# Kernel tuning notes

Measured on AMD Instinct MI355X. Metric: run time of the kernel, lower is better.

## Reference

```python
import jax, jax.numpy as jnp
import numpy as np

D_K = 64


def setup_inputs() -> dict:
    key = jax.random.key(0)
    kq, kk, kv = jax.random.split(key, 3)
    B, H, S, D = 2, 16, 2048, D_K
    Q = jax.random.normal(kq, (B, H, S, D), dtype=jnp.float32)
    K = jax.random.normal(kk, (B, H, S, D), dtype=jnp.float32)
    V = jax.random.normal(kv, (B, H, S, D), dtype=jnp.float32)
    # causal mask: True = masked out (matches torch masked_fill_ semantics)
    causal = ~jnp.tril(jnp.ones((S, S), dtype=bool))
    attn_mask = jnp.broadcast_to(causal, (B, 1, S, S))
    return {"Q": Q, "K": K, "V": V, "attn_mask": attn_mask}


def reference(Q, K, V, attn_mask):
    # scores = Q K^T / sqrt(d_k), masked positions -> -1e9, softmax, then A V
    scale = 1.0 / np.sqrt(D_K).astype(np.float32)
    scores = jnp.einsum("bhqd,bhkd->bhqk", Q, K) * scale
    scores = jnp.where(attn_mask, jnp.float32(-1e9), scores)
    attn = jax.nn.softmax(scores, axis=-1)
    context = jnp.einsum("bhqk,bhkd->bhqd", attn, V)
    return (context, attn)
```

## Files before the change

kernel.cpp:

```cpp
#include <hip/hip_runtime.h>

typedef _Float16 half8  __attribute__((ext_vector_type(8)));
typedef _Float16 half4v __attribute__((ext_vector_type(4)));
typedef float    f32x4  __attribute__((ext_vector_type(4)));

#define S_LEN  2048
#define D_HEAD 64
#define TQ     16
#define EBS    2056

static __device__ __forceinline__ half8 cvt8(float4 a, float4 b) {
    half8 h;
    h[0] = (_Float16)a.x; h[1] = (_Float16)a.y; h[2] = (_Float16)a.z; h[3] = (_Float16)a.w;
    h[4] = (_Float16)b.x; h[5] = (_Float16)b.y; h[6] = (_Float16)b.z; h[7] = (_Float16)b.w;
    return h;
}

__global__ void prep_k(const float* __restrict__ K, _Float16* __restrict__ Kh, int n8) {
    int i = blockIdx.x * blockDim.x + threadIdx.x;
    if (i < n8) {
        const float4* p = (const float4*)K + (size_t)i * 2;
        ((half8*)Kh)[i] = cvt8(p[0], p[1]);
    }
}

__global__ void prep_vt(const float* __restrict__ V, _Float16* __restrict__ Vt) {
    __shared__ _Float16 lt[D_HEAD][136];
    const int bh = blockIdx.y;
    const int k0 = blockIdx.x * 128;
    const int t  = threadIdx.x;
    {
        const int kk = t >> 1, hf = t & 1;
        const float* vp = V + (size_t)bh * S_LEN * D_HEAD + (size_t)(k0 + kk) * D_HEAD + hf * 32;
#pragma unroll
        for (int j = 0; j < 8; ++j) {
            float4 a = *(const float4*)(vp + j * 4);
            lt[hf * 32 + j * 4 + 0][kk] = (_Float16)a.x;
            lt[hf * 32 + j * 4 + 1][kk] = (_Float16)a.y;
            lt[hf * 32 + j * 4 + 2][kk] = (_Float16)a.z;
            lt[hf * 32 + j * 4 + 3][kk] = (_Float16)a.w;
        }
    }
    __syncthreads();
    {
        const int d = t >> 2, kq = t & 3;
        _Float16* dst = Vt + ((size_t)bh * D_HEAD + d) * S_LEN + k0 + kq * 32;
        const half8* src = (const half8*)&lt[d][kq * 32];
#pragma unroll
        for (int j = 0; j < 4; ++j) ((half8*)dst)[j] = src[j];
    }
}

template <bool USE_WS>
__global__ __launch_bounds__(256, 2)
void sdpa_main(const float* __restrict__ Q, const float* __restrict__ K,
               const _Float16* __restrict__ Kh, const float* __restrict__ V,
               const _Float16* __restrict__ Vt, float* __restrict__ ctx,
               float* __restrict__ attn) {
    __shared__ __align__(16) _Float16 ebuf[TQ][EBS];
    __shared__ float rowsum[TQ];
    __shared__ float inv_l[TQ];

    const int tid  = threadIdx.x;
    const int wave = tid >> 6;
    const int lane = tid & 63;
    const int c    = lane & 15;
    const int quad = lane >> 4;

    const int qt = blockIdx.x;
    const int bh = blockIdx.y;
    const int q0 = qt * TQ;
    const int n_k   = q0 + TQ;
    const int n_t16 = n_k >> 4;
    const int n_c32 = (n_k + 31) >> 5;

    const size_t base = (size_t)bh * (S_LEN * D_HEAD);

    if (tid < TQ) rowsum[tid] = 0.0f;
    if (n_k & 31) {
        int r = tid >> 4, kk = n_k + (tid & 15);
        ebuf[r][kk] = (_Float16)0.0f;
    }

    half8 qf0, qf1;
    {
        const float* qp = Q + base + (size_t)(q0 + c) * D_HEAD + quad * 8;
        qf0 = cvt8(*(const float4*)qp, *(const float4*)(qp + 4));
        qf1 = cvt8(*(const float4*)(qp + 32), *(const float4*)(qp + 36));
    }
    __syncthreads();

    float psum = 0.0f;
    for (int t = wave; t < n_t16; t += 4) {
        const int k0 = t * 16;
        half8 kf0, kf1;
        if (USE_WS) {
            const _Float16* kp = Kh + base + (size_t)(k0 + c) * D_HEAD + quad * 8;
            kf0 = *(const half8*)kp;
            kf1 = *(const half8*)(kp + 32);
        } else {
            const float* kp = K + base + (size_t)(k0 + c) * D_HEAD + quad * 8;
            kf0 = cvt8(*(const float4*)kp, *(const float4*)(kp + 4));
            kf1 = cvt8(*(const float4*)(kp + 32), *(const float4*)(kp + 36));
        }
        f32x4 s = {0.0f, 0.0f, 0.0f, 0.0f};
        s = __builtin_amdgcn_mfma_f32_16x16x32_f16(kf0, qf0, s, 0, 0, 0);
        s = __builtin_amdgcn_mfma_f32_16x16x32_f16(kf1, qf1, s, 0, 0, 0);

        half4v ev;
#pragma unroll
        for (int r = 0; r < 4; ++r) {
            const int kg = k0 + quad * 4 + r;
            float e = (kg <= q0 + c) ? __expf(s[r] * 0.125f) : 0.0f;
            psum += e;
            ev[r] = (_Float16)e;
        }
        *(half4v*)&ebuf[c][k0 + quad * 4] = ev;
    }
    psum += __shfl_xor(psum, 16);
    psum += __shfl_xor(psum, 32);
    if (lane < 16) atomicAdd(&rowsum[c], psum);
    __syncthreads();
    if (tid < TQ) inv_l[tid] = 1.0f / rowsum[tid];

    f32x4 cacc = {0.0f, 0.0f, 0.0f, 0.0f};
    if (USE_WS) {
        const _Float16* vb = Vt + ((size_t)bh * D_HEAD + wave * 16 + c) * S_LEN;
        for (int chk = 0; chk < n_c32; ++chk) {
            const int k0 = chk * 32;
            half8 af = *(const half8*)&ebuf[c][k0 + quad * 8];
            half8 bf = *(const half8*)(vb + k0 + quad * 8);
            cacc = __builtin_amdgcn_mfma_f32_16x16x32_f16(af, bf, cacc, 0, 0, 0);
        }
    } else {
        for (int chk = 0; chk < n_c32; ++chk) {
            const int k0 = chk * 32;
            half8 af = *(const half8*)&ebuf[c][k0 + quad * 8];
            half8 bf;
#pragma unroll
            for (int j = 0; j < 8; ++j)
                bf[j] = (_Float16)V[base + (size_t)(k0 + quad * 8 + j) * D_HEAD + wave * 16 + c];
            cacc = __builtin_amdgcn_mfma_f32_16x16x32_f16(af, bf, cacc, 0, 0, 0);
        }
    }
    __syncthreads();

    {
        const int r  = tid >> 4;
        const int qg = q0 + r;
        const float il = inv_l[r];
        float* row = attn + (size_t)bh * S_LEN * S_LEN + (size_t)(q0 + r) * S_LEN;
#pragma unroll
        for (int it = 0; it < 16; ++it) {
            const int k8 = (tid & 15) * 8 + it * 128;
            float4 o0, o1;
            if (k8 + 7 <= qg) {
                half8 e = *(const half8*)&ebuf[r][k8];
                o0.x = (float)e[0] * il; o0.y = (float)e[1] * il;
                o0.z = (float)e[2] * il; o0.w = (float)e[3] * il;
                o1.x = (float)e[4] * il; o1.y = (float)e[5] * il;
                o1.z = (float)e[6] * il; o1.w = (float)e[7] * il;
            } else if (k8 > qg) {
                o0.x = o0.y = o0.z = o0.w = 0.0f;
                o1 = o0;
            } else {
                half8 e = *(const half8*)&ebuf[r][k8];
                o0.x = (k8 + 0 <= qg) ? (float)e[0] * il : 0.0f;
                o0.y = (k8 + 1 <= qg) ? (float)e[1] * il : 0.0f;
                o0.z = (k8 + 2 <= qg) ? (float)e[2] * il : 0.0f;
                o0.w = (k8 + 3 <= qg) ? (float)e[3] * il : 0.0f;
                o1.x = (k8 + 4 <= qg) ? (float)e[4] * il : 0.0f;
                o1.y = (k8 + 5 <= qg) ? (float)e[5] * il : 0.0f;
                o1.z = (k8 + 6 <= qg) ? (float)e[6] * il : 0.0f;
                o1.w = (k8 + 7 <= qg) ? (float)e[7] * il : 0.0f;
            }
            *(float4*)(row + k8)     = o0;
            *(float4*)(row + k8 + 4) = o1;
        }
    }

#pragma unroll
    for (int r = 0; r < 4; ++r) {
        const int qr = quad * 4 + r;
        ctx[base + (size_t)(q0 + qr) * D_HEAD + wave * 16 + c] = cacc[r] * inv_l[qr];
    }
}

extern "C" void kernel_launch(void* const* d_in, const int* in_sizes, int n_in,
                              void* d_out, int out_size, void* d_ws, size_t ws_size,
                              hipStream_t stream) {
    const float* Q = (const float*)d_in[0];
    const float* K = (const float*)d_in[1];
    const float* V = (const float*)d_in[2];

    const int BH = in_sizes[0] / (S_LEN * D_HEAD);
    float* ctx  = (float*)d_out;
    float* attn = (float*)d_out + (size_t)in_sizes[0];

    const size_t nKV  = (size_t)in_sizes[1];
    const size_t need = 2 * nKV * sizeof(_Float16);

    dim3 grid(S_LEN / TQ, BH);
    if (ws_size >= need) {
        _Float16* Kh = (_Float16*)d_ws;
        _Float16* Vt = Kh + nKV;
        prep_k<<<(int)((nKV / 8 + 255) / 256), 256, 0, stream>>>(K, Kh, (int)(nKV / 8));
        prep_vt<<<dim3(S_LEN / 128, BH), 256, 0, stream>>>(V, Vt);
        sdpa_main<true><<<grid, 256, 0, stream>>>(Q, K, Kh, V, Vt, ctx, attn);
    } else {
        sdpa_main<false><<<grid, 256, 0, stream>>>(Q, K, nullptr, V, nullptr, ctx, attn);
    }
}
```

Before: 744.9 us.

## Fuse K/V prep, schedule heavy tiles first, interleave PV MFMA with attn stores

Merges the K conversion and V transpose prep kernels into one launch. Remaps the flattened grid so the longest causal query tiles start first, with heads spread across the grid. Interleaves the P·V MFMA chunks with the streaming attention-matrix writes and makes those writes nontemporal. The aim is to hide the large attn store traffic behind compute and cut tail imbalance, at the cost of a hardcoded BH==32 grid mapping and a more complex loop.

```diff
diff --git a/kernel.cpp b/kernel.cpp
--- a/kernel.cpp
+++ b/kernel.cpp
@@ -16,19 +16,37 @@
     return h;
 }
 
-__global__ void prep_k(const float* __restrict__ K, _Float16* __restrict__ Kh, int n8) {
-    int i = blockIdx.x * blockDim.x + threadIdx.x;
-    if (i < n8) {
-        const float4* p = (const float4*)K + (size_t)i * 2;
-        ((half8*)Kh)[i] = cvt8(p[0], p[1]);
-    }
-}
-
-__global__ void prep_vt(const float* __restrict__ V, _Float16* __restrict__ Vt) {
+static __device__ __forceinline__ f32x4 attn_seg(const _Float16* er, int kb, int qg, float il) {
+    f32x4 o;
+    if (kb > qg) { o[0] = o[1] = o[2] = o[3] = 0.0f; return o; }
+    half4v e = *(const half4v*)(er + kb);
+    if (kb + 3 <= qg) {
+        o[0] = (float)e[0] * il; o[1] = (float)e[1] * il;
+        o[2] = (float)e[2] * il; o[3] = (float)e[3] * il;
+    } else {
+        o[0] = (float)e[0] * il;
+        o[1] = (kb + 1 <= qg) ? (float)e[1] * il : 0.0f;
+        o[2] = (kb + 2 <= qg) ? (float)e[2] * il : 0.0f;
+        o[3] = (kb + 3 <= qg) ? (float)e[3] * il : 0.0f;
+    }
+    return o;
+}
+
+__global__ void prep_kv(const float* __restrict__ K, _Float16* __restrict__ Kh,
+                        const float* __restrict__ V, _Float16* __restrict__ Vt) {
     __shared__ _Float16 lt[D_HEAD][136];
     const int bh = blockIdx.y;
     const int k0 = blockIdx.x * 128;
     const int t  = threadIdx.x;
+    {
+        const size_t b8 = ((size_t)bh * S_LEN + k0) * D_HEAD / 8;
+#pragma unroll
+        for (int j = 0; j < 4; ++j) {
+            const size_t i = b8 + t + j * 256;
+            const float4* p = (const float4*)K + i * 2;
+            ((half8*)Kh)[i] = cvt8(p[0], p[1]);
+        }
+    }
     {
         const int kk = t >> 1, hf = t & 1;
         const float* vp = V + (size_t)bh * S_LEN * D_HEAD + (size_t)(k0 + kk) * D_HEAD + hf * 32;
@@ -59,7 +77,6 @@
                float* __restrict__ attn) {
     __shared__ __align__(16) _Float16 ebuf[TQ][EBS];
     __shared__ float rowsum[TQ];
-    __shared__ float inv_l[TQ];
 
     const int tid  = threadIdx.x;
     const int wave = tid >> 6;
@@ -67,8 +84,16 @@
     const int c    = lane & 15;
     const int quad = lane >> 4;
 
-    const int qt = blockIdx.x;
-    const int bh = blockIdx.y;
+    int qt, bh;
+    if (gridDim.y == 1) {
+        const int f = blockIdx.x;
+        bh = ((f & 7) << 2) | ((f >> 3) & 3);
+        qt = 127 - (f >> 5);
+    } else {
+        qt = blockIdx.x;
+        bh = blockIdx.y;
+    }
+
     const int q0 = qt * TQ;
     const int n_k   = q0 + TQ;
     const int n_t16 = n_k >> 4;
@@ -121,68 +146,49 @@
     psum += __shfl_xor(psum, 32);
     if (lane < 16) atomicAdd(&rowsum[c], psum);
     __syncthreads();
-    if (tid < TQ) inv_l[tid] = 1.0f / rowsum[tid];
 
     f32x4 cacc = {0.0f, 0.0f, 0.0f, 0.0f};
-    if (USE_WS) {
-        const _Float16* vb = Vt + ((size_t)bh * D_HEAD + wave * 16 + c) * S_LEN;
-        for (int chk = 0; chk < n_c32; ++chk) {
-            const int k0 = chk * 32;
-            half8 af = *(const half8*)&ebuf[c][k0 + quad * 8];
-            half8 bf = *(const half8*)(vb + k0 + quad * 8);
-            cacc = __builtin_amdgcn_mfma_f32_16x16x32_f16(af, bf, cacc, 0, 0, 0);
-        }
-    } else {
-        for (int chk = 0; chk < n_c32; ++chk) {
-            const int k0 = chk * 32;
-            half8 af = *(const half8*)&ebuf[c][k0 + quad * 8];
-            half8 bf;
-#pragma unroll
-            for (int j = 0; j < 8; ++j)
-                bf[j] = (_Float16)V[base + (size_t)(k0 + quad * 8 + j) * D_HEAD + wave * 16 + c];
-            cacc = __builtin_amdgcn_mfma_f32_16x16x32_f16(af, bf, cacc, 0, 0, 0);
-        }
-    }
-    __syncthreads();
-
     {
         const int r  = tid >> 4;
+        const int c4 = (tid & 15) * 4;
         const int qg = q0 + r;
-        const float il = inv_l[r];
-        float* row = attn + (size_t)bh * S_LEN * S_LEN + (size_t)(q0 + r) * S_LEN;
+        const float il = 1.0f / rowsum[r];
+        const _Float16* er = ebuf[r];
+        float* rowp = attn + (size_t)bh * S_LEN * S_LEN + (size_t)qg * S_LEN;
+        const _Float16* vb = USE_WS
+            ? Vt + ((size_t)bh * D_HEAD + wave * 16 + c) * S_LEN
+            : nullptr;
+
+        int chk = 0;
 #pragma unroll
         for (int it = 0; it < 16; ++it) {
-            const int k8 = (tid & 15) * 8 + it * 128;
-            float4 o0, o1;
-            if (k8 + 7 <= qg) {
-                half8 e = *(const half8*)&ebuf[r][k8];
-                o0.x = (float)e[0] * il; o0.y = (float)e[1] * il;
-                o0.z = (float)e[2] * il; o0.w = (float)e[3] * il;
-                o1.x = (float)e[4] * il; o1.y = (float)e[5] * il;
-                o1.z = (float)e[6] * il; o1.w = (float)e[7] * il;
-            } else if (k8 > qg) {
-                o0.x = o0.y = o0.z = o0.w = 0.0f;
-                o1 = o0;
-            } else {
-                half8 e = *(const half8*)&ebuf[r][k8];
-                o0.x = (k8 + 0 <= qg) ? (float)e[0] * il : 0.0f;
-                o0.y = (k8 + 1 <= qg) ? (float)e[1] * il : 0.0f;
-                o0.z = (k8 + 2 <= qg) ? (float)e[2] * il : 0.0f;
-                o0.w = (k8 + 3 <= qg) ? (float)e[3] * il : 0.0f;
-                o1.x = (k8 + 4 <= qg) ? (float)e[4] * il : 0.0f;
-                o1.y = (k8 + 5 <= qg) ? (float)e[5] * il : 0.0f;
-                o1.z = (k8 + 6 <= qg) ? (float)e[6] * il : 0.0f;
-                o1.w = (k8 + 7 <= qg) ? (float)e[7] * il : 0.0f;
+            const int lim = ((it + 1) * n_c32) >> 4;
+            for (; chk < lim; ++chk) {
+                const int k0 = chk * 32;
+                half8 af = *(const half8*)&ebuf[c][k0 + quad * 8];
+                half8 bf;
+                if (USE_WS) {
+                    bf = *(const half8*)(vb + k0 + quad * 8);
+                } else {
+#pragma unroll
+                    for (int j = 0; j < 8; ++j)
+                        bf[j] = (_Float16)V[base + (size_t)(k0 + quad * 8 + j) * D_HEAD + wave * 16 + c];
+                }
+                cacc = __builtin_amdgcn_mfma_f32_16x16x32_f16(af, bf, cacc, 0, 0, 0);
             }
-            *(float4*)(row + k8)     = o0;
-            *(float4*)(row + k8 + 4) = o1;
-        }
-    }
-
-#pragma unroll
-    for (int r = 0; r < 4; ++r) {
-        const int qr = quad * 4 + r;
-        ctx[base + (size_t)(q0 + qr) * D_HEAD + wave * 16 + c] = cacc[r] * inv_l[qr];
+            const int colA = it * 128 + c4;
+            const int colB = colA + 64;
+            f32x4 oA = attn_seg(er, colA, qg, il);
+            f32x4 oB = attn_seg(er, colB, qg, il);
+            __builtin_nontemporal_store(oA, (f32x4*)(rowp + colA));
+            __builtin_nontemporal_store(oB, (f32x4*)(rowp + colB));
+        }
+    }
+
+#pragma unroll
+    for (int rr = 0; rr < 4; ++rr) {
+        const int qr = quad * 4 + rr;
+        ctx[base + (size_t)(q0 + qr) * D_HEAD + wave * 16 + c] = cacc[rr] * (1.0f / rowsum[qr]);
     }
 }
 
@@ -200,14 +206,16 @@
     const size_t nKV  = (size_t)in_sizes[1];
     const size_t need = 2 * nKV * sizeof(_Float16);
 
-    dim3 grid(S_LEN / TQ, BH);
     if (ws_size >= need) {
         _Float16* Kh = (_Float16*)d_ws;
         _Float16* Vt = Kh + nKV;
-        prep_k<<<(int)((nKV / 8 + 255) / 256), 256, 0, stream>>>(K, Kh, (int)(nKV / 8));
-        prep_vt<<<dim3(S_LEN / 128, BH), 256, 0, stream>>>(V, Vt);
-        sdpa_main<true><<<grid, 256, 0, stream>>>(Q, K, Kh, V, Vt, ctx, attn);
+        prep_kv<<<dim3(S_LEN / 128, BH), 256, 0, stream>>>(K, Kh, V, Vt);
+        if (BH == 32) {
+            sdpa_main<true><<<dim3((S_LEN / TQ) * BH, 1), 256, 0, stream>>>(Q, K, Kh, V, Vt, ctx, attn);
+        } else {
+            sdpa_main<true><<<dim3(S_LEN / TQ, BH), 256, 0, stream>>>(Q, K, Kh, V, Vt, ctx, attn);
+        }
     } else {
-        sdpa_main<false><<<grid, 256, 0, stream>>>(Q, K, nullptr, V, nullptr, ctx, attn);
-    }
-}
+        sdpa_main<false><<<dim3(S_LEN / TQ, BH), 256, 0, stream>>>(Q, K, nullptr, V, nullptr, ctx, attn);
+    }
+}
```

Result: faster. 688.4 us (-7.6%).
